# Performance work log

Measured on AMD Instinct MI355X. Metric: run time of the kernel, lower is better.

Reference implementation:

```python
import jax, jax.numpy as jnp
import numpy as np

B, S, T = 4, 1024, 2048
HID = 1024
NH = 16
NKV = 4
HD = HID // NH  # 64


def setup_inputs() -> dict:
    key = jax.random.key(0)
    ks = jax.random.split(key, 6)
    scale = 1.0 / np.sqrt(HID)
    return {
        "x": jax.random.normal(ks[0], (B, S, HID), dtype=jnp.float32),
        "context": jax.random.normal(ks[1], (B, T, HID), dtype=jnp.float32),
        "Wq": jax.random.normal(ks[2], (NH * HD, HID), dtype=jnp.float32) * scale,
        "Wk": jax.random.normal(ks[3], (NKV * HD, HID), dtype=jnp.float32) * scale,
        "Wv": jax.random.normal(ks[4], (NKV * HD, HID), dtype=jnp.float32) * scale,
        "Wo": jax.random.normal(ks[5], (HID, NH * HD), dtype=jnp.float32) * scale,
    }


def reference(x, context, Wq, Wk, Wv, Wo):
    Bx, Sx, _ = x.shape
    Tx = context.shape[1]
    rep = NH // NKV
    # projections (Linear with no bias: y = x @ W.T)
    q = (x @ Wq.T).reshape(Bx, Sx, NKV, rep, HD)          # group query heads by KV head
    k = (context @ Wk.T).reshape(Bx, Tx, NKV, HD)
    v = (context @ Wv.T).reshape(Bx, Tx, NKV, HD)
    scale = 1.0 / jnp.sqrt(jnp.asarray(HD, dtype=q.dtype))
    # scores: [B, NKV, rep, S, T] -- shares K across the rep grouped heads
    # (math-identical to repeat_interleave then SDPA, without materializing K/V copies)
    scores = jnp.einsum("bsgrd,btgd->bgrst", q, k) * scale
    attn = jax.nn.softmax(scores, axis=-1)
    out = jnp.einsum("bgrst,btgd->bsgrd", attn, v)        # [B,S,NKV,rep,HD]
    out = out.reshape(Bx, Sx, NH * HD)
    return out @ Wo.T
```

## Files before the change

kernel.cpp:

```cpp
#include <hip/hip_runtime.h>
#include <hip/hip_bf16.h>
#include <stdint.h>

typedef __bf16 bf16x8 __attribute__((ext_vector_type(8)));
typedef _Float16 f16x8 __attribute__((ext_vector_type(8)));
typedef _Float16 f16x2 __attribute__((ext_vector_type(2)));
typedef float f32x4 __attribute__((ext_vector_type(4)));
typedef unsigned short u16;
typedef unsigned int u32;

struct __align__(8) us4 { u16 x, y, z, w; };

#define LOG2E 1.44269504088896f
#define QSCALE (0.125f * LOG2E)

__device__ __forceinline__ void async_load16(const void* g, void* l) {
    __builtin_amdgcn_global_load_lds(
        (const __attribute__((address_space(1))) u32*)(uintptr_t)g,
        (__attribute__((address_space(3))) u32*)(u32)(uintptr_t)l,
        16, 0, 0);
}

__device__ __forceinline__ u16 f2bfbits(float f) {
    __bf16 h = (__bf16)f;
    return __builtin_bit_cast(u16, h);
}
__device__ __forceinline__ u16 f2hbits(float f) {
    _Float16 h = (_Float16)f;
    return __builtin_bit_cast(u16, h);
}
__device__ __forceinline__ f16x2 pkrtz(float a, float b) {
    return __builtin_bit_cast(f16x2, __builtin_amdgcn_cvt_pkrtz(a, b));
}

__device__ __forceinline__ bf16x8 frag_from_f32(const float* T, int row, int kkq2, int id) {
    const float4 lo = *(const float4*)&T[row * 64 + (((kkq2) ^ id) << 2)];
    const float4 hi = *(const float4*)&T[row * 64 + (((kkq2 + 1) ^ id) << 2)];
    bf16x8 f;
    f[0] = (__bf16)lo.x; f[1] = (__bf16)lo.y; f[2] = (__bf16)lo.z; f[3] = (__bf16)lo.w;
    f[4] = (__bf16)hi.x; f[5] = (__bf16)hi.y; f[6] = (__bf16)hi.z; f[7] = (__bf16)hi.w;
    return f;
}

__global__ __launch_bounds__(256) void proj_qkv(
    const float* __restrict__ x, const float* __restrict__ ctx,
    const float* __restrict__ Wq, const float* __restrict__ Wk,
    const float* __restrict__ Wv,
    u16* __restrict__ q, u16* __restrict__ k2, u16* __restrict__ vT) {
    __shared__ float As[128 * 64];
    __shared__ float Bs[128 * 64];
    const int tid = threadIdx.x;
    const int w = tid >> 6, lane = tid & 63, quad = lane >> 4, id = lane & 15;
    const int wr = (w >> 1) * 64, wc = (w & 1) * 64;
    const int arow = lane >> 4;
    const int swzcb = (lane & 15) ^ (w * 4 + arow);

    const int bid = blockIdx.x;
    const float *A, *Bm;
    int mtile, ntile, mode;
    if (bid < 256) {
        mode = 0; A = x; Bm = Wq;
        mtile = (bid >> 3) * 128; ntile = (bid & 7) * 128;
    } else if (bid < 384) {
        int s2 = bid - 256;
        mode = 1; A = ctx; Bm = Wk;
        mtile = (s2 >> 1) * 128; ntile = (s2 & 1) * 128;
    } else {
        int s2 = bid - 384;
        mode = 2; A = ctx; Bm = Wv;
        mtile = (s2 >> 1) * 128; ntile = (s2 & 1) * 128;
    }

    f32x4 acc[4][4];
#pragma unroll
    for (int i = 0; i < 4; i++)
#pragma unroll
        for (int j = 0; j < 4; j++) acc[i][j] = (f32x4){0.f, 0.f, 0.f, 0.f};

    for (int k0 = 0; k0 < 1024; k0 += 64) {
        __syncthreads();
#pragma unroll
        for (int is = 0; is < 8; is++) {
            int base = is * 16 + w * 4;
            async_load16(A + (size_t)(mtile + base + arow) * 1024 + k0 + swzcb * 4,
                         &As[base * 64]);
        }
#pragma unroll
        for (int is = 0; is < 8; is++) {
            int base = is * 16 + w * 4;
            async_load16(Bm + (size_t)(ntile + base + arow) * 1024 + k0 + swzcb * 4,
                         &Bs[base * 64]);
        }
        __syncthreads();
#pragma unroll
        for (int kk = 0; kk < 2; kk++) {
            const int kkq2 = kk * 8 + quad * 2;
            bf16x8 af[4], bfr[4];
#pragma unroll
            for (int i = 0; i < 4; i++)
                af[i] = frag_from_f32(As, wr + i * 16 + id, kkq2, id);
#pragma unroll
            for (int j = 0; j < 4; j++)
                bfr[j] = frag_from_f32(Bs, wc + j * 16 + id, kkq2, id);
#pragma unroll
            for (int i = 0; i < 4; i++)
#pragma unroll
                for (int j = 0; j < 4; j++)
                    acc[i][j] = __builtin_amdgcn_mfma_f32_16x16x32_bf16(af[i], bfr[j], acc[i][j], 0, 0, 0);
        }
    }

#pragma unroll
    for (int i = 0; i < 4; i++)
#pragma unroll
        for (int j = 0; j < 4; j++) {
            int mbase = mtile + wr + i * 16 + quad * 4;
            int n = ntile + wc + j * 16 + id;
            if (mode == 2) {
                int b = mbase >> 11, t = mbase & 2047;
                int g = n >> 6, d = n & 63;
                us4 pk;
                pk.x = f2hbits(acc[i][j][0]);
                pk.y = f2hbits(acc[i][j][1]);
                pk.z = f2hbits(acc[i][j][2]);
                pk.w = f2hbits(acc[i][j][3]);
                *(us4*)&vT[((size_t)((b << 2) + g) * 64 + d) * 2048 + t] = pk;
            } else if (mode == 1) {
#pragma unroll
                for (int r = 0; r < 4; r++) {
                    int m = mbase + r;
                    int b = m >> 11, t = m & 2047;
                    int g = n >> 6, d = n & 63;
                    k2[((size_t)((b << 2) + g) * 2048 + t) * 64 + d] = f2bfbits(acc[i][j][r]);
                }
            } else {
#pragma unroll
                for (int r = 0; r < 4; r++)
                    q[(size_t)(mbase + r) * 1024 + n] = f2bfbits(acc[i][j][r] * QSCALE);
            }
        }
}

__global__ __launch_bounds__(256) void gemm_out(const u16* __restrict__ A,
                                                const float* __restrict__ Bm,
                                                float* __restrict__ C) {
    __shared__ u16 As[128 * 64];
    __shared__ float Bs[128 * 64];
    const int tid = threadIdx.x;
    const int w = tid >> 6, lane = tid & 63, quad = lane >> 4, id = lane & 15;
    const int mtile = blockIdx.y * 128, ntile = blockIdx.x * 128;
    const int wr = (w >> 1) * 64, wc = (w & 1) * 64;
    const int arow = lane >> 4;
    const int swzcb = (lane & 15) ^ (w * 4 + arow);
    const int stgswz8 = ((lane & 7) ^ (lane >> 3)) * 8;

    f32x4 acc[4][4];
#pragma unroll
    for (int i = 0; i < 4; i++)
#pragma unroll
        for (int j = 0; j < 4; j++) acc[i][j] = (f32x4){0.f, 0.f, 0.f, 0.f};

    for (int k0 = 0; k0 < 1024; k0 += 64) {
        __syncthreads();
#pragma unroll
        for (int is = 0; is < 4; is++) {
            int base = is * 32 + w * 8;
            async_load16(A + (size_t)(mtile + base + (lane >> 3)) * 1024 + k0 + stgswz8,
                         &As[base * 64]);
        }
#pragma unroll
        for (int is = 0; is < 8; is++) {
            int base = is * 16 + w * 4;
            async_load16(Bm + (size_t)(ntile + base + arow) * 1024 + k0 + swzcb * 4,
                         &Bs[base * 64]);
        }
        __syncthreads();
#pragma unroll
        for (int kk = 0; kk < 2; kk++) {
            const int kkq2 = kk * 8 + quad * 2;
            bf16x8 af[4], bfr[4];
#pragma unroll
            for (int i = 0; i < 4; i++) {
                int row = wr + i * 16 + id;
                af[i] = *(const bf16x8*)&As[row * 64 + (((kk * 4 + quad) ^ (id & 7)) * 8)];
            }
#pragma unroll
            for (int j = 0; j < 4; j++)
                bfr[j] = frag_from_f32(Bs, wc + j * 16 + id, kkq2, id);
#pragma unroll
            for (int i = 0; i < 4; i++)
#pragma unroll
                for (int j = 0; j < 4; j++)
                    acc[i][j] = __builtin_amdgcn_mfma_f32_16x16x32_bf16(af[i], bfr[j], acc[i][j], 0, 0, 0);
        }
    }

#pragma unroll
    for (int i = 0; i < 4; i++)
#pragma unroll
        for (int j = 0; j < 4; j++) {
            int mbase = mtile + wr + i * 16 + quad * 4;
            int n = ntile + wc + j * 16 + id;
#pragma unroll
            for (int r = 0; r < 4; r++)
                C[(size_t)(mbase + r) * 1024 + n] = acc[i][j][r];
        }
}

__global__ __launch_bounds__(256, 2) void attn_kernel(const u16* __restrict__ q,
                                                      const u16* __restrict__ k2,
                                                      const u16* __restrict__ vT,
                                                      u16* __restrict__ o) {
    __shared__ u16 Ks[2][64 * 64];
    __shared__ u16 Vt[2][64 * 64];
    const int tid = threadIdx.x;
    const int w = tid >> 6, lane = tid & 63, quad = lane >> 4, id = lane & 15;

    const int bid = blockIdx.x;
    const int xcd = bid & 7, slot = bid >> 3;
    const int bg = xcd * 2 + (slot >> 5);
    const int inner = slot & 31;
    const int b = bg >> 2, g = bg & 3;
    const int h = g * 4 + (inner >> 3);
    const int s0 = (inner & 7) * 128;

    const int stgswz = (((lane & 7) ^ (lane >> 3) ^ ((w & 1) << 2))) * 8;
    int kfkey[2];
#pragma unroll
    for (int c = 0; c < 2; c++)
        kfkey[c] = (id & 3) | (((c ^ ((id >> 2) & 1)) & 1) << 2);
    const int vkey = (id & 7) ^ (((id >> 3) & 1) << 2);
    const int trow_base = ((id & 12) << 1) + (id & 3);

    bf16x8 qf[2][2];
#pragma unroll
    for (int rb = 0; rb < 2; rb++) {
        const size_t base = ((size_t)(b * 1024 + s0 + w * 32 + rb * 16 + id)) * 1024 + h * 64;
        qf[rb][0] = *(const bf16x8*)&q[base + quad * 8];
        qf[rb][1] = *(const bf16x8*)&q[base + 32 + quad * 8];
    }

    f16x8 ones;
#pragma unroll
    for (int i = 0; i < 8; i++) ones[i] = (_Float16)1.0f;

    f32x4 acc[2][4], accl[2];
#pragma unroll
    for (int rb = 0; rb < 2; rb++) {
        accl[rb] = (f32x4){0.f, 0.f, 0.f, 0.f};
#pragma unroll
        for (int i = 0; i < 4; i++) acc[rb][i] = (f32x4){0.f, 0.f, 0.f, 0.f};
    }

    const size_t kbase = ((size_t)(b * 4 + g)) * 2048 * 64;
    const size_t vbase = ((size_t)(b * 4 + g)) * 64 * 2048;

    auto stage = [&](int t0, int buf) {
#pragma unroll
        for (int is = 0; is < 2; is++) {
            int tl = is * 32 + w * 8;
            async_load16(&k2[kbase + (size_t)(t0 + tl + (lane >> 3)) * 64 + stgswz],
                         &Ks[buf][tl * 64]);
        }
#pragma unroll
        for (int is = 0; is < 2; is++) {
            int dl = is * 32 + w * 8;
            async_load16(&vT[vbase + (size_t)(dl + (lane >> 3)) * 2048 + t0 + stgswz],
                         &Vt[buf][dl * 64]);
        }
    };

    stage(0, 0);
    __syncthreads();

    int cur = 0;
    for (int t0 = 0; t0 < 2048; t0 += 64) {
        if (t0 + 64 < 2048) stage(t0 + 64, cur ^ 1);

        f32x4 s[2][2][2];
#pragma unroll
        for (int kk = 0; kk < 2; kk++)
#pragma unroll
            for (int P = 0; P < 2; P++)
#pragma unroll
                for (int c = 0; c < 2; c++) {
                    int trow = P * 32 + trow_base + c * 4;
                    bf16x8 kf = *(const bf16x8*)&Ks[cur][trow * 64 + (((kk * 4 + quad) ^ kfkey[c]) * 8)];
#pragma unroll
                    for (int rb = 0; rb < 2; rb++)
                        s[rb][P][c] = __builtin_amdgcn_mfma_f32_16x16x32_bf16(
                            kf, qf[rb][kk],
                            kk ? s[rb][P][c] : (f32x4){0.f, 0.f, 0.f, 0.f}, 0, 0, 0);
                }

        f16x8 pa[2][2];
        union PU { f16x8 v; f16x2 h[4]; };
#pragma unroll
        for (int rb = 0; rb < 2; rb++)
#pragma unroll
            for (int P = 0; P < 2; P++) {
                PU u;
#pragma unroll
                for (int c = 0; c < 2; c++) {
                    float e0 = __builtin_exp2f(s[rb][P][c][0]);
                    float e1 = __builtin_exp2f(s[rb][P][c][1]);
                    float e2 = __builtin_exp2f(s[rb][P][c][2]);
                    float e3 = __builtin_exp2f(s[rb][P][c][3]);
                    u.h[c * 2 + 0] = pkrtz(e0, e1);
                    u.h[c * 2 + 1] = pkrtz(e2, e3);
                }
                pa[rb][P] = u.v;
            }

#pragma unroll
        for (int P = 0; P < 2; P++) {
#pragma unroll
            for (int db = 0; db < 4; db++) {
                f16x8 vf = *(const f16x8*)&Vt[cur][(db * 16 + id) * 64 + (((P * 4 + quad) ^ vkey) * 8)];
#pragma unroll
                for (int rb = 0; rb < 2; rb++)
                    acc[rb][db] = __builtin_amdgcn_mfma_f32_16x16x32_f16(pa[rb][P], vf, acc[rb][db], 0, 0, 0);
            }
#pragma unroll
            for (int rb = 0; rb < 2; rb++)
                accl[rb] = __builtin_amdgcn_mfma_f32_16x16x32_f16(pa[rb][P], ones, accl[rb], 0, 0, 0);
        }

        __syncthreads();
        cur ^= 1;
    }

#pragma unroll
    for (int rb = 0; rb < 2; rb++) {
        f32x4 inv;
#pragma unroll
        for (int r = 0; r < 4; r++) inv[r] = 1.0f / accl[rb][r];
#pragma unroll
        for (int db = 0; db < 4; db++)
#pragma unroll
            for (int r = 0; r < 4; r++) {
                int srow = s0 + w * 32 + rb * 16 + quad * 4 + r;
                o[((size_t)(b * 1024 + srow)) * 1024 + h * 64 + db * 16 + id] =
                    f2bfbits(acc[rb][db][r] * inv[r]);
            }
    }
}

extern "C" void kernel_launch(void* const* d_in, const int* in_sizes, int n_in,
                              void* d_out, int out_size, void* d_ws, size_t ws_size,
                              hipStream_t stream) {
    (void)in_sizes; (void)n_in; (void)out_size; (void)ws_size;
    const float* x   = (const float*)d_in[0];
    const float* ctx = (const float*)d_in[1];
    const float* Wq  = (const float*)d_in[2];
    const float* Wk  = (const float*)d_in[3];
    const float* Wv  = (const float*)d_in[4];
    const float* Wo  = (const float*)d_in[5];
    float* out = (float*)d_out;

    u16* q  = (u16*)d_ws;
    u16* k2 = q + 4096 * 1024;
    u16* vT = k2 + 4 * 4 * 2048 * 64;
    u16* o  = vT + 4 * 4 * 64 * 2048;

    proj_qkv<<<512, 256, 0, stream>>>(x, ctx, Wq, Wk, Wv, q, k2, vT);
    attn_kernel<<<512, 256, 0, stream>>>(q, k2, vT, o);
    gemm_out<<<dim3(8, 32), 256, 0, stream>>>(o, Wo, out);
}
```

Before: 215.1 us.

## Split attention KV range in two with partial outputs and combine kernel

Splits the 2048-length key/value sequence into two halves handled by separate blocks, doubling the attention grid to 1024 blocks and raising occupancy to 4 blocks per CU. Each block writes unnormalised fp32 partial outputs and row sums, and a new combine kernel adds the two halves, normalises and converts to bf16. The staging loop is also restructured into an unrolled ping-pong with pointer increments. This trades extra global traffic (two fp32 partial buffers) and a kernel launch for more parallelism and latency hiding. It relies on there being no running max, so partials combine by plain addition.

```diff
diff --git a/kernel.cpp b/kernel.cpp
--- a/kernel.cpp
+++ b/kernel.cpp
@@ -207,10 +207,11 @@
         }
 }
 
-__global__ __launch_bounds__(256, 2) void attn_kernel(const u16* __restrict__ q,
+__global__ __launch_bounds__(256, 4) void attn_kernel(const u16* __restrict__ q,
                                                       const u16* __restrict__ k2,
                                                       const u16* __restrict__ vT,
-                                                      u16* __restrict__ o) {
+                                                      float* __restrict__ opart,
+                                                      float* __restrict__ lpart) {
     __shared__ u16 Ks[2][64 * 64];
     __shared__ u16 Vt[2][64 * 64];
     const int tid = threadIdx.x;
@@ -218,11 +219,14 @@
 
     const int bid = blockIdx.x;
     const int xcd = bid & 7, slot = bid >> 3;
-    const int bg = xcd * 2 + (slot >> 5);
-    const int inner = slot & 31;
+    const int bg = xcd * 2 + (slot >> 6);
+    const int inner = slot & 63;
+    const int th = inner >> 5;
+    const int hs = inner & 31;
     const int b = bg >> 2, g = bg & 3;
-    const int h = g * 4 + (inner >> 3);
-    const int s0 = (inner & 7) * 128;
+    const int h = g * 4 + (hs >> 3);
+    const int s0 = (hs & 7) * 128;
+    const int tstart = th * 1024;
 
     const int stgswz = (((lane & 7) ^ (lane >> 3) ^ ((w & 1) << 2))) * 8;
     int kfkey[2];
@@ -252,31 +256,21 @@
         for (int i = 0; i < 4; i++) acc[rb][i] = (f32x4){0.f, 0.f, 0.f, 0.f};
     }
 
-    const size_t kbase = ((size_t)(b * 4 + g)) * 2048 * 64;
-    const size_t vbase = ((size_t)(b * 4 + g)) * 64 * 2048;
-
-    auto stage = [&](int t0, int buf) {
-#pragma unroll
-        for (int is = 0; is < 2; is++) {
-            int tl = is * 32 + w * 8;
-            async_load16(&k2[kbase + (size_t)(t0 + tl + (lane >> 3)) * 64 + stgswz],
-                         &Ks[buf][tl * 64]);
-        }
-#pragma unroll
-        for (int is = 0; is < 2; is++) {
-            int dl = is * 32 + w * 8;
-            async_load16(&vT[vbase + (size_t)(dl + (lane >> 3)) * 2048 + t0 + stgswz],
-                         &Vt[buf][dl * 64]);
-        }
+    const u16* kp = k2 + ((size_t)(b * 4 + g)) * 2048 * 64
+                  + (size_t)(tstart + w * 8 + (lane >> 3)) * 64 + stgswz;
+    const u16* vp = vT + ((size_t)(b * 4 + g)) * 64 * 2048
+                  + (size_t)(w * 8 + (lane >> 3)) * 2048 + tstart + stgswz;
+
+    auto stage = [&](int buf) {
+        async_load16(kp,             &Ks[buf][(w * 8) * 64]);
+        async_load16(kp + 32 * 64,   &Ks[buf][(32 + w * 8) * 64]);
+        async_load16(vp,             &Vt[buf][(w * 8) * 64]);
+        async_load16(vp + 32 * 2048, &Vt[buf][(32 + w * 8) * 64]);
+        kp += 64 * 64;
+        vp += 64;
     };
 
-    stage(0, 0);
-    __syncthreads();
-
-    int cur = 0;
-    for (int t0 = 0; t0 < 2048; t0 += 64) {
-        if (t0 + 64 < 2048) stage(t0 + 64, cur ^ 1);
-
+    auto process = [&](const u16* Ksb, const u16* Vtb) {
         f32x4 s[2][2][2];
 #pragma unroll
         for (int kk = 0; kk < 2; kk++)
@@ -285,7 +279,7 @@
 #pragma unroll
                 for (int c = 0; c < 2; c++) {
                     int trow = P * 32 + trow_base + c * 4;
-                    bf16x8 kf = *(const bf16x8*)&Ks[cur][trow * 64 + (((kk * 4 + quad) ^ kfkey[c]) * 8)];
+                    bf16x8 kf = *(const bf16x8*)&Ksb[trow * 64 + (((kk * 4 + quad) ^ kfkey[c]) * 8)];
 #pragma unroll
                     for (int rb = 0; rb < 2; rb++)
                         s[rb][P][c] = __builtin_amdgcn_mfma_f32_16x16x32_bf16(
@@ -316,7 +310,7 @@
         for (int P = 0; P < 2; P++) {
 #pragma unroll
             for (int db = 0; db < 4; db++) {
-                f16x8 vf = *(const f16x8*)&Vt[cur][(db * 16 + id) * 64 + (((P * 4 + quad) ^ vkey) * 8)];
+                f16x8 vf = *(const f16x8*)&Vtb[(db * 16 + id) * 64 + (((P * 4 + quad) ^ vkey) * 8)];
 #pragma unroll
                 for (int rb = 0; rb < 2; rb++)
                     acc[rb][db] = __builtin_amdgcn_mfma_f32_16x16x32_f16(pa[rb][P], vf, acc[rb][db], 0, 0, 0);
@@ -325,25 +319,62 @@
             for (int rb = 0; rb < 2; rb++)
                 accl[rb] = __builtin_amdgcn_mfma_f32_16x16x32_f16(pa[rb][P], ones, accl[rb], 0, 0, 0);
         }
-
-        __syncthreads();
-        cur ^= 1;
-    }
-
-#pragma unroll
-    for (int rb = 0; rb < 2; rb++) {
-        f32x4 inv;
-#pragma unroll
-        for (int r = 0; r < 4; r++) inv[r] = 1.0f / accl[rb][r];
+    };
+
+    stage(0);
+    __syncthreads();
+
+#pragma unroll 1
+    for (int it = 0; it < 8; ++it) {
+        stage(1);
+        process(Ks[0], Vt[0]);
+        __syncthreads();
+        if (it != 7) stage(0);
+        process(Ks[1], Vt[1]);
+        __syncthreads();
+    }
+
+    float* op = opart + (size_t)th * (4096 * 1024);
+    float* lp = lpart + (size_t)th * (4096 * 16);
+#pragma unroll
+    for (int rb = 0; rb < 2; rb++)
 #pragma unroll
         for (int db = 0; db < 4; db++)
 #pragma unroll
             for (int r = 0; r < 4; r++) {
                 int srow = s0 + w * 32 + rb * 16 + quad * 4 + r;
-                o[((size_t)(b * 1024 + srow)) * 1024 + h * 64 + db * 16 + id] =
-                    f2bfbits(acc[rb][db][r] * inv[r]);
-            }
-    }
+                op[((size_t)(b * 1024 + srow)) * 1024 + h * 64 + db * 16 + id] = acc[rb][db][r];
+            }
+    if (id == 0) {
+#pragma unroll
+        for (int rb = 0; rb < 2; rb++)
+#pragma unroll
+            for (int r = 0; r < 4; r++) {
+                int srow = s0 + w * 32 + rb * 16 + quad * 4 + r;
+                lp[(size_t)(b * 1024 + srow) * 16 + h] = accl[rb][r];
+            }
+    }
+}
+
+__global__ __launch_bounds__(256) void combine_kernel(const float* __restrict__ opart,
+                                                      const float* __restrict__ lpart,
+                                                      u16* __restrict__ o) {
+    int i = blockIdx.x * 256 + threadIdx.x;
+    int m = i >> 7;
+    int n0 = (i & 127) * 8;
+    int hh = n0 >> 6;
+    float inv = 1.0f / (lpart[(size_t)m * 16 + hh] + lpart[4096 * 16 + (size_t)m * 16 + hh]);
+    const float* p0 = opart + (size_t)m * 1024 + n0;
+    const float* p1 = p0 + (size_t)4096 * 1024;
+    float4 a0 = *(const float4*)p0, a1 = *(const float4*)(p0 + 4);
+    float4 b0 = *(const float4*)p1, b1 = *(const float4*)(p1 + 4);
+    us4 lo, hi;
+    lo.x = f2bfbits((a0.x + b0.x) * inv); lo.y = f2bfbits((a0.y + b0.y) * inv);
+    lo.z = f2bfbits((a0.z + b0.z) * inv); lo.w = f2bfbits((a0.w + b0.w) * inv);
+    hi.x = f2bfbits((a1.x + b1.x) * inv); hi.y = f2bfbits((a1.y + b1.y) * inv);
+    hi.z = f2bfbits((a1.z + b1.z) * inv); hi.w = f2bfbits((a1.w + b1.w) * inv);
+    *(us4*)&o[(size_t)m * 1024 + n0] = lo;
+    *(us4*)&o[(size_t)m * 1024 + n0 + 4] = hi;
 }
 
 extern "C" void kernel_launch(void* const* d_in, const int* in_sizes, int n_in,
@@ -358,12 +389,15 @@
     const float* Wo  = (const float*)d_in[5];
     float* out = (float*)d_out;
 
-    u16* q  = (u16*)d_ws;
-    u16* k2 = q + 4096 * 1024;
-    u16* vT = k2 + 4 * 4 * 2048 * 64;
-    u16* o  = vT + 4 * 4 * 64 * 2048;
+    u16*   q     = (u16*)d_ws;
+    u16*   k2    = q + 4096 * 1024;
+    u16*   vT    = k2 + 4 * 4 * 2048 * 64;
+    u16*   o     = vT + 4 * 4 * 64 * 2048;
+    float* opart = (float*)(o + 4096 * 1024);
+    float* lpart = opart + 2 * 4096 * 1024;
 
     proj_qkv<<<512, 256, 0, stream>>>(x, ctx, Wq, Wk, Wv, q, k2, vT);
-    attn_kernel<<<512, 256, 0, stream>>>(q, k2, vT, o);
+    attn_kernel<<<1024, 256, 0, stream>>>(q, k2, vT, opart, lpart);
+    combine_kernel<<<2048, 256, 0, stream>>>(opart, lpart, o);
     gemm_out<<<dim3(8, 32), 256, 0, stream>>>(o, Wo, out);
 }
```

Result: slower. 221.2 us (+2.8%).
